# Kernel tuning notes

Hardware: AMD Instinct MI355X
Metric: run time of the kernel (lower is better)

The kernel has to match this reference:

```python
import jax, jax.numpy as jnp
import numpy as np
import math

BS, SEQ = 2048, 50
REL, ETYPE = 6, 4
ATT, HEADS, HEAD = 64, 4, 16
HID, OUT = 128, 64


def setup_inputs() -> dict:
    key = jax.random.key(0)
    ks = jax.random.split(key, 20)
    d = {}
    d['input_seqs'] = jax.random.normal(ks[0], (BS, SEQ, 3, 3, REL), jnp.float32)
    d['input_edge_types'] = jax.random.uniform(ks[1], (BS, SEQ, 3, 3, ETYPE), jnp.float32)
    d['input_masks'] = jax.random.randint(ks[2], (BS, SEQ, 3, 3), 0, 2, jnp.int32)
    def lin(k, fin, fout):
        k1, k2 = jax.random.split(k)
        bound = 1.0 / math.sqrt(fin)
        W = jax.random.uniform(k1, (fout, fin), jnp.float32, -bound, bound)
        b = jax.random.uniform(k2, (fout,), jnp.float32, -bound, bound)
        return W, b
    d['W_fus'], d['b_fus'] = lin(ks[3], REL + ETYPE + 9, 64)
    d['Wk'], d['bk'] = lin(ks[4], REL, ATT)
    d['Wq'], d['bq'] = lin(ks[5], 64, ATT)
    d['Wv'], d['bv'] = lin(ks[6], 64, ATT)
    bound = 1.0 / math.sqrt(HID)
    d['W_ih'] = jax.random.uniform(ks[7], (4 * HID, ATT), jnp.float32, -bound, bound)
    d['W_hh'] = jax.random.uniform(ks[8], (4 * HID, HID), jnp.float32, -bound, bound)
    d['b_ih'] = jax.random.uniform(ks[9], (4 * HID,), jnp.float32, -bound, bound)
    d['b_hh'] = jax.random.uniform(ks[10], (4 * HID,), jnp.float32, -bound, bound)
    d['W_out'], d['b_out'] = lin(ks[11], HID, OUT)
    return d


def _lstm_last(xs, W_ih, W_hh, b_ih, b_hh):
    # xs: (seq, bs, ATT); torch LSTM gate order i,f,g,o. Returns last hidden state.
    b = b_ih + b_hh
    def step(carry, x):
        h, c = carry
        gates = x @ W_ih.T + h @ W_hh.T + b
        i, f, g, o = jnp.split(gates, 4, axis=-1)
        i, f, o = jax.nn.sigmoid(i), jax.nn.sigmoid(f), jax.nn.sigmoid(o)
        g = jnp.tanh(g)
        c = f * c + i * g
        h = o * jnp.tanh(c)
        return (h, c), None
    h0 = jnp.zeros((xs.shape[1], HID), xs.dtype)
    (h, _), _ = jax.lax.scan(step, (h0, h0), xs)
    return h


def reference(input_seqs, input_edge_types, input_masks, W_fus, b_fus, Wk, bk, Wq, bq, Wv, bv, W_ih, W_hh, b_ih, b_hh, W_out, b_out):
    bs, seq = input_seqs.shape[0], input_seqs.shape[1]
    # location one-hot for the 3x3 neighborhood
    loc = jnp.broadcast_to(jnp.eye(9, dtype=input_seqs.dtype).reshape(3, 3, 9), (bs, seq, 3, 3, 9))
    edge_info = jnp.concatenate([input_seqs, input_edge_types, loc], axis=-1)
    edge_info = edge_info @ W_fus.T + b_fus                 # (bs, seq, 3, 3, 64)
    edge_info = edge_info.reshape(bs, seq, 9, 64)
    self_info = input_seqs[:, :, 1, 1]                       # (bs, seq, REL)
    # key from self state (same for all 9 slots), query/value from edge info
    key = (self_info @ Wk.T + bk).reshape(bs, seq, 1, HEADS, HEAD)     # broadcast over 9
    query = (edge_info @ Wq.T + bq).reshape(bs, seq, 9, HEADS, HEAD)
    value = (edge_info @ Wv.T + bv).reshape(bs, seq, 9, HEADS, HEAD)
    # att: dot over head dim -> (bs, seq, heads, 9)
    att = jnp.einsum('bsnhd,bsnhd->bshn', jnp.broadcast_to(key, query.shape), query) / math.sqrt(HEAD)
    mask9 = input_masks.reshape(bs, seq, 1, 9)               # broadcast over heads
    att = jnp.where(mask9 == 0, jnp.float32(-1e10), att)
    att = jax.nn.softmax(att, axis=-1)                       # (bs, seq, heads, 9)
    ctx = jnp.einsum('bshn,bsnhd->bshd', att, value)         # (bs, seq, heads, head)
    ctx = ctx.reshape(bs, seq, ATT).transpose(1, 0, 2)       # (seq, bs, ATT)
    h_last = _lstm_last(ctx, W_ih, W_hh, b_ih, b_hh)         # (bs, HID)
    return h_last @ W_out.T + b_out                          # (bs, OUT)
```

## Files before the change

### kernel.cpp

```cpp
#include <hip/hip_runtime.h>
#include <math.h>

#define BS   2048
#define SEQ  50
#define NPOS (BS * SEQ)

typedef __attribute__((ext_vector_type(8))) short bf16x8;
typedef __attribute__((ext_vector_type(4))) float f32x4;

__device__ __forceinline__ float sigf(float x) { return 1.0f / (1.0f + __expf(-x)); }
__device__ __forceinline__ float tanhfast(float x) {
    float e = __expf(2.0f * x);
    return 1.0f - 2.0f / (e + 1.0f);
}
__device__ __forceinline__ unsigned short bfrn(float x) {
    unsigned int u = __float_as_uint(x);
    u += 0x7FFFu + ((u >> 16) & 1u);
    return (unsigned short)(u >> 16);
}
__device__ __forceinline__ float bf2f(unsigned short h) {
    return __uint_as_float(((unsigned int)h) << 16);
}

#define FMA4(A, X, W) \
    A = fmaf((X).x, (W).x, A); A = fmaf((X).y, (W).y, A); \
    A = fmaf((X).z, (W).z, A); A = fmaf((X).w, (W).w, A);

__device__ float Wvf_d[640];
__device__ float Ce_d[576];
__device__ float Ag_d[280];
__device__ float Bd_d[252];

__global__ __launch_bounds__(512) void prep_all(
    const float* __restrict__ Wih, const float* __restrict__ Whh,
    bf16x8* __restrict__ whF, bf16x8* __restrict__ wiF,
    const float* __restrict__ Wf, const float* __restrict__ bf,
    const float* __restrict__ Wq, const float* __restrict__ bq,
    const float* __restrict__ Wv,
    const float* __restrict__ Wk, const float* __restrict__ bk)
{
    int id = blockIdx.x * 512 + threadIdx.x;
    if (id < 24576) {
        const float* src;
        bf16x8* dst;
        int p;
        if (id < 16384) {
            int l = id & 63, frag = id >> 6;
            p = frag & 1;
            int kc = (frag >> 1) & 3, ti = (frag >> 3) & 3, w = frag >> 5;
            int n  = (w + 8 * ti) * 16 + (l & 15);
            int k0 = kc * 32 + (l >> 4) * 8;
            src = &Whh[n * 128 + k0];
            dst = &whF[frag * 64 + l];
        } else {
            int id2 = id - 16384;
            int l = id2 & 63, frag = id2 >> 6;
            p = frag & 1;
            int kc = (frag >> 1) & 1, tile = frag >> 2;
            int n  = tile * 16 + (l & 15);
            int k0 = kc * 32 + (l >> 4) * 8;
            src = &Wih[n * 64 + k0];
            dst = &wiF[frag * 64 + l];
        }
        bf16x8 v;
        #pragma unroll
        for (int j = 0; j < 8; ++j) {
            float x = src[j];
            unsigned short hi = bfrn(x);
            unsigned short r  = p ? bfrn(x - bf2f(hi)) : hi;
            v[j] = (short)r;
        }
        *dst = v;
        return;
    }
    int i = id - 24576;
    if (i >= 1748) return;
    if (i < 640) {
        int o = i / 10, k = i % 10;
        float s = 0.f;
        #pragma unroll 8
        for (int j = 0; j < 64; ++j) s = fmaf(Wv[o * 64 + j], Wf[j * 19 + k], s);
        Wvf_d[i] = s;
    } else if (i < 1216) {
        int i2 = i - 640;
        int o = i2 / 9, e = i2 % 9;
        float s = 0.f;
        #pragma unroll 8
        for (int j = 0; j < 64; ++j)
            s = fmaf(Wf[j * 19 + 10 + e] + bf[j], Wv[o * 64 + j], s);
        Ce_d[i2] = s;
    } else if (i < 1496) {
        int i3 = i - 1216;
        int h = i3 / 70, rem = i3 % 70, k = rem / 7, j = rem % 7;
        float s = 0.f;
        for (int d = 0; d < 16; ++d) {
            int n = h * 16 + d;
            float Gnk = 0.f;
            #pragma unroll 8
            for (int mm = 0; mm < 64; ++mm)
                Gnk = fmaf(Wq[n * 64 + mm], Wf[mm * 19 + k], Gnk);
            float wkj = (j < 6) ? Wk[n * 6 + j] : bk[n];
            s = fmaf(wkj, Gnk, s);
        }
        Ag_d[i3] = s;
    } else {
        int i4 = i - 1496;
        int e = i4 / 28, rem = i4 % 28, h = rem / 7, j = rem % 7;
        float s = 0.f;
        for (int d = 0; d < 16; ++d) {
            int n = h * 16 + d;
            float Den = bq[n];
            #pragma unroll 8
            for (int mm = 0; mm < 64; ++mm)
                Den = fmaf(Wf[mm * 19 + 10 + e] + bf[mm], Wq[n * 64 + mm], Den);
            float wkj = (j < 6) ? Wk[n * 6 + j] : bk[n];
            s = fmaf(wkj, Den, s);
        }
        Bd_d[i4] = s;
    }
}

__global__ __launch_bounds__(64, 4) void edge_attn_ctx(
    const float* __restrict__ seqs,
    const float* __restrict__ ets,
    const int*   __restrict__ masks,
    const float* __restrict__ bv,
    float* __restrict__ ctx)
{
    const int o   = threadIdx.x;
    const int h_o = o >> 4;
    const int lg  = (o < 40) ? o : 0;
    const int gh  = lg / 10, gk = lg % 10;
    const int la  = (o < 36) ? o : 0;
    const int ah  = la / 9,  ae = la % 9;

    float Agr[7], Bdr[7];
    #pragma unroll
    for (int j = 0; j < 7; ++j) Agr[j] = Ag_d[(gh * 10 + gk) * 7 + j];
    #pragma unroll
    for (int j = 0; j < 7; ++j) Bdr[j] = Bd_d[(ae * 4 + ah) * 7 + j];
    float Wvfr[10];
    #pragma unroll
    for (int k = 0; k < 10; ++k) Wvfr[k] = Wvf_d[o * 10 + k];
    const float bvr = bv[o];
    float Cer[9];
    #pragma unroll
    for (int e = 0; e < 9; ++e) Cer[e] = Ce_d[o * 9 + e] + bvr;

    __shared__ float s_seq[54], s_et[36], s_g[40];
    __shared__ float s_att[36], s_exp[36], s_rbar[40];
    __shared__ int   s_mask[9];

    float r_seq = 0.f, r_et = 0.f; int r_mask = 0;
    {
        int p0 = blockIdx.x;
        if (o < 54) r_seq  = seqs[p0 * 54 + o];
        if (o < 36) r_et   = ets[p0 * 36 + o];
        if (o < 9)  r_mask = masks[p0 * 9 + o];
    }

    for (int p = blockIdx.x; p < NPOS; p += gridDim.x) {
        if (o < 54) s_seq[o]  = r_seq;
        if (o < 36) s_et[o]   = r_et;
        if (o < 9)  s_mask[o] = r_mask;
        __syncthreads();

        {
            int pn = p + gridDim.x;
            if (pn < NPOS) {
                if (o < 54) r_seq  = seqs[pn * 54 + o];
                if (o < 36) r_et   = ets[pn * 36 + o];
                if (o < 9)  r_mask = masks[pn * 9 + o];
            }
        }

        float c0 = s_seq[24], c1 = s_seq[25], c2 = s_seq[26],
              c3 = s_seq[27], c4 = s_seq[28], c5 = s_seq[29];
        float tt = 0.f;
        if (o < 40) {
            float g = Agr[6];
            g = fmaf(c0, Agr[0], g); g = fmaf(c1, Agr[1], g);
            g = fmaf(c2, Agr[2], g); g = fmaf(c3, Agr[3], g);
            g = fmaf(c4, Agr[4], g); g = fmaf(c5, Agr[5], g);
            s_g[o] = g;
        }
        if (o < 36) {
            tt = Bdr[6];
            tt = fmaf(c0, Bdr[0], tt); tt = fmaf(c1, Bdr[1], tt);
            tt = fmaf(c2, Bdr[2], tt); tt = fmaf(c3, Bdr[3], tt);
            tt = fmaf(c4, Bdr[4], tt); tt = fmaf(c5, Bdr[5], tt);
        }
        __syncthreads();

        float a = 0.f;
        if (o < 36) {
            a = tt;
            #pragma unroll
            for (int k = 0; k < 6; ++k) a = fmaf(s_seq[ae * 6 + k], s_g[ah * 10 + k], a);
            #pragma unroll
            for (int k = 0; k < 4; ++k) a = fmaf(s_et[ae * 4 + k], s_g[ah * 10 + 6 + k], a);
            a *= 0.25f;
            if (s_mask[ae] == 0) a = -1.0e10f;
            s_att[o] = a;
        }
        __syncthreads();

        float ex = 0.f;
        if (o < 36) {
            float mx = s_att[ah * 9 + 0];
            #pragma unroll
            for (int e = 1; e < 9; ++e) mx = fmaxf(mx, s_att[ah * 9 + e]);
            ex = __expf(a - mx);
            s_exp[o] = ex;
        }
        __syncthreads();

        if (o < 40) {
            float rb = 0.f;
            #pragma unroll
            for (int e = 0; e < 9; ++e) {
                float x = (gk < 6) ? s_seq[e * 6 + gk] : s_et[e * 4 + (gk - 6)];
                rb = fmaf(s_exp[gh * 9 + e], x, rb);
            }
            s_rbar[o] = rb;
        }
        __syncthreads();

        {
            float ssum = 0.f;
            #pragma unroll
            for (int e = 0; e < 9; ++e) ssum += s_exp[h_o * 9 + e];
            float acc = 0.f;
            #pragma unroll
            for (int k = 0; k < 10; ++k) acc = fmaf(s_rbar[h_o * 10 + k], Wvfr[k], acc);
            #pragma unroll
            for (int e = 0; e < 9; ++e) acc = fmaf(s_exp[h_o * 9 + e], Cer[e], acc);
            ctx[p * 64 + o] = acc * (1.0f / ssum);
        }
        __syncthreads();
    }
}

#define MFMA16(A, B, C) __builtin_amdgcn_mfma_f32_16x16x32_bf16(A, B, C, 0, 0, 0)
#define MM4(F, W0, W1, W2, W3) \
    a0 = MFMA16(F, W0, a0); a1 = MFMA16(F, W1, a1); \
    a2 = MFMA16(F, W2, a2); a3 = MFMA16(F, W3, a3);

#define HPASS \
    MM4(hfh[0], whr[0][0][0], whr[1][0][0], whr[2][0][0], whr[3][0][0]) \
    MM4(hfh[1], whr[0][1][0], whr[1][1][0], whr[2][1][0], whr[3][1][0]) \
    MM4(hfh[2], whr[0][2][0], whr[1][2][0], whr[2][2][0], whr[3][2][0]) \
    MM4(hfh[3], whr[0][3][0], whr[1][3][0], whr[2][3][0], whr[3][3][0]) \
    MM4(hfl[0], whr[0][0][0], whr[1][0][0], whr[2][0][0], whr[3][0][0]) \
    MM4(hfl[1], whr[0][1][0], whr[1][1][0], whr[2][1][0], whr[3][1][0]) \
    MM4(hfl[2], whr[0][2][0], whr[1][2][0], whr[2][2][0], whr[3][2][0]) \
    MM4(hfl[3], whr[0][3][0], whr[1][3][0], whr[2][3][0], whr[3][3][0]) \
    MM4(hfh[0], whr[0][0][1], whr[1][0][1], whr[2][0][1], whr[3][0][1]) \
    MM4(hfh[1], whr[0][1][1], whr[1][1][1], whr[2][1][1], whr[3][1][1]) \
    MM4(hfh[2], whr[0][2][1], whr[1][2][1], whr[2][2][1], whr[3][2][1]) \
    MM4(hfh[3], whr[0][3][1], whr[1][3][1], whr[2][3][1], whr[3][3][1])

#define REDIST_E(ch, g0, g1) { \
    float s2_ = __shfl_xor(ch[2], 32), s3_ = __shfl_xor(ch[3], 32); \
    g0 = lolq ? ch[0] : s2_;  g1 = lolq ? ch[1] : s3_; }
#define REDIST_O(ch, g0, g1) { \
    float s0_ = __shfl_xor(ch[0], 32), s1_ = __shfl_xor(ch[1], 32); \
    g0 = lolq ? s0_ : ch[2];  g1 = lolq ? s1_ : ch[3]; }

#define PWBODY(gi0,gf0,gg0,go0,gi1,gf1,gg1,go1, WB0, WB1) { \
    float i0_ = sigf(gi0 + bi), f0_ = sigf(gf0 + bff); \
    float gA_ = tanhfast(gg0 + bg), o0_ = sigf(go0 + bo); \
    c20 = fmaf(f0_, c20, i0_ * gA_); \
    float hv0_ = o0_ * tanhfast(c20); \
    float i1_ = sigf(gi1 + bi), f1_ = sigf(gf1 + bff); \
    float gB_ = tanhfast(gg1 + bg), o1_ = sigf(go1 + bo); \
    c21 = fmaf(f1_, c21, i1_ * gB_); \
    float hv1_ = o1_ * tanhfast(c21); \
    unsigned short hh0_ = bfrn(hv0_), hh1_ = bfrn(hv1_); \
    unsigned short hl0_ = bfrn(hv0_ - bf2f(hh0_)), hl1_ = bfrn(hv1_ - bf2f(hh1_)); \
    *(unsigned short*)((char*)s_hh + (WB0)) = hh0_; \
    *(unsigned short*)((char*)s_hl + (WB0)) = hl0_; \
    *(unsigned short*)((char*)s_hh + (WB1)) = hh1_; \
    *(unsigned short*)((char*)s_hl + (WB1)) = hl1_; }

__global__ __launch_bounds__(512, 2) void lstm_mfma(
    const float*  __restrict__ ctx,
    const bf16x8* __restrict__ whF,
    const bf16x8* __restrict__ wiFg,
    const float*  __restrict__ b_ih, const float* __restrict__ b_hh,
    const float*  __restrict__ W_out, const float* __restrict__ b_out,
    float* __restrict__ out)
{
    const int t  = threadIdx.x;
    const int w  = t >> 6, l = t & 63;
    const int lm = l & 15, lq = l >> 4;
    const int row0 = blockIdx.x * 8;

    __shared__ bf16x8 s_wi[8192];
    __shared__ unsigned short s_xh[1024], s_xl[1024];
    __shared__ unsigned short s_hh[4096], s_hl[4096];

    for (int i = t; i < 8192; i += 512) s_wi[i] = wiFg[i];
    for (int i = t; i < 1024; i += 512) { s_xh[i] = 0; s_xl[i] = 0; }
    for (int i = t; i < 4096; i += 512) { s_hh[i] = 0; s_hl[i] = 0; }

    bf16x8 whr[4][4][2];
    #pragma unroll
    for (int ti = 0; ti < 4; ++ti)
        #pragma unroll
        for (int kc = 0; kc < 4; ++kc)
            #pragma unroll
            for (int p = 0; p < 2; ++p)
                whr[ti][kc][p] = whF[(((w * 4 + ti) * 4 + kc) * 2 + p) * 64 + l];

    const int m = w * 16 + lm;
    const float bi  = b_ih[m]       + b_hh[m];
    const float bff = b_ih[128 + m] + b_hh[128 + m];
    const float bg  = b_ih[256 + m] + b_hh[256 + m];
    const float bo  = b_ih[384 + m] + b_hh[384 + m];

    const int  urb  = ((lq & 1) << 2) | (lq & 2);
    const bool lolq = (lq < 2);
    float c20 = 0.f, c21 = 0.f;

    const int xrow  = t >> 5;
    const int xl32  = t & 31;
    const int srow  = xrow & 7;
    const int spair = xrow >> 3;
    const float2* ctx2 = (const float2*)ctx;
    const int xbase = (row0 + srow) * SEQ + spair;
    const int xwb   = xrow * 128 + ((4 * xl32) ^ ((xrow & 7) << 4));
    const int swzr  = (lm & 7) << 4;
    const int hwb_m = 32 * w + 2 * lm;
    const int wb0e = 4096 + (8 + urb) * 256 + (hwb_m ^ (urb << 4));
    const int wb1e = 4096 + (9 + urb) * 256 + (hwb_m ^ ((urb + 1) << 4));
    const int wb0o = urb * 256 + (hwb_m ^ (urb << 4));
    const int wb1o = (urb + 1) * 256 + (hwb_m ^ ((urb + 1) << 4));

    float2 xv = ctx2[xbase * 32 + xl32];

    for (int u = 0; u < SEQ / 2; ++u) {
        {
            unsigned short xh0 = bfrn(xv.x), xh1 = bfrn(xv.y);
            unsigned short xl0 = bfrn(xv.x - bf2f(xh0)), xl1 = bfrn(xv.y - bf2f(xh1));
            *(unsigned int*)((char*)s_xh + xwb) = (unsigned int)xh0 | ((unsigned int)xh1 << 16);
            *(unsigned int*)((char*)s_xl + xwb) = (unsigned int)xl0 | ((unsigned int)xl1 << 16);
        }
        __syncthreads();

        float2 xvn = make_float2(0.f, 0.f);
        if (u + 1 < SEQ / 2) xvn = ctx2[(xbase + 2 * u + 2) * 32 + xl32];

        bf16x8 hfh[4], hfl[4];
        if (u > 0) {
            #pragma unroll
            for (int kc = 0; kc < 4; ++kc) {
                int b = lm * 256 + ((kc * 64 + lq * 16) ^ swzr);
                hfh[kc] = *(const bf16x8*)((const char*)s_hh + b);
                hfl[kc] = *(const bf16x8*)((const char*)s_hl + b);
            }
        }
        bf16x8 xfh[2], xfl[2];
        #pragma unroll
        for (int kc = 0; kc < 2; ++kc) {
            int b = lm * 128 + ((kc * 64 + lq * 16) ^ swzr);
            xfh[kc] = *(const bf16x8*)((const char*)s_xh + b);
            xfl[kc] = *(const bf16x8*)((const char*)s_xl + b);
        }

        f32x4 a0 = {0.f,0.f,0.f,0.f}, a1 = a0, a2 = a0, a3 = a0;

        if (u > 0) { HPASS }

        #pragma unroll
        for (int kc = 0; kc < 2; ++kc) {
            bf16x8 wihi[4], wilo[4];
            #pragma unroll
            for (int ti = 0; ti < 4; ++ti) {
                int base = (((w + 8 * ti) * 2 + kc) * 2) * 64 + l;
                wihi[ti] = s_wi[base];
                wilo[ti] = s_wi[base + 64];
            }
            MM4(xfh[kc], wihi[0], wihi[1], wihi[2], wihi[3])
            MM4(xfl[kc], wihi[0], wihi[1], wihi[2], wihi[3])
            MM4(xfh[kc], wilo[0], wilo[1], wilo[2], wilo[3])
        }

        {
            float gi0, gi1, gf0, gf1, gg0, gg1, go0, go1;
            REDIST_E(a0, gi0, gi1)
            REDIST_E(a1, gf0, gf1)
            REDIST_E(a2, gg0, gg1)
            REDIST_E(a3, go0, go1)
            PWBODY(gi0, gf0, gg0, go0, gi1, gf1, gg1, go1, wb0e, wb1e)
        }

        __syncthreads();
        #pragma unroll
        for (int kc = 0; kc < 4; ++kc) {
            int b = 4096 + lm * 256 + ((kc * 64 + lq * 16) ^ swzr);
            hfh[kc] = *(const bf16x8*)((const char*)s_hh + b);
            hfl[kc] = *(const bf16x8*)((const char*)s_hl + b);
        }
        HPASS

        {
            float gi0, gi1, gf0, gf1, gg0, gg1, go0, go1;
            REDIST_O(a0, gi0, gi1)
            REDIST_O(a1, gf0, gf1)
            REDIST_O(a2, gg0, gg1)
            REDIST_O(a3, go0, go1)
            PWBODY(gi0, gf0, gg0, go0, gi1, gf1, gg1, go1, wb0o, wb1o)
        }
        xv = xvn;
    }
    __syncthreads();

    {
        const int row = t >> 5;
        if (row < 8) {
            const int j0 = t & 31, j1 = (t & 31) + 32;
            const int rswz = (row & 7) << 4;
            float accA = b_out[j0], accB = b_out[j1];
            #pragma unroll
            for (int kq = 0; kq < 16; ++kq) {
                int b = row * 256 + ((kq * 16) ^ rswz);
                bf16x8 hh8 = *(const bf16x8*)((const char*)s_hh + b);
                bf16x8 hl8 = *(const bf16x8*)((const char*)s_hl + b);
                #pragma unroll
                for (int e = 0; e < 8; ++e) {
                    float h = bf2f((unsigned short)hh8[e]) + bf2f((unsigned short)hl8[e]);
                    int k = kq * 8 + e;
                    accA = fmaf(h, W_out[j0 * 128 + k], accA);
                    accB = fmaf(h, W_out[j1 * 128 + k], accB);
                }
            }
            out[(row0 + row) * 64 + j0] = accA;
            out[(row0 + row) * 64 + j1] = accB;
        }
    }
}

extern "C" void kernel_launch(void* const* d_in, const int* in_sizes, int n_in,
                              void* d_out, int out_size, void* d_ws, size_t ws_size,
                              hipStream_t stream) {
    (void)in_sizes; (void)n_in; (void)out_size; (void)ws_size;
    const float* seqs  = (const float*)d_in[0];
    const float* ets   = (const float*)d_in[1];
    const int*   masks = (const int*)d_in[2];
    const float* Wf  = (const float*)d_in[3];
    const float* bf  = (const float*)d_in[4];
    const float* Wk  = (const float*)d_in[5];
    const float* bk  = (const float*)d_in[6];
    const float* Wq  = (const float*)d_in[7];
    const float* bq  = (const float*)d_in[8];
    const float* Wv  = (const float*)d_in[9];
    const float* bv  = (const float*)d_in[10];
    const float* Wih = (const float*)d_in[11];
    const float* Whh = (const float*)d_in[12];
    const float* bih = (const float*)d_in[13];
    const float* bhh = (const float*)d_in[14];
    const float* Wo  = (const float*)d_in[15];
    const float* bo  = (const float*)d_in[16];

    char* ws = (char*)d_ws;
    bf16x8* whF = (bf16x8*)(ws);
    bf16x8* wiF = (bf16x8*)(ws + 262144);
    float*  ctx = (float*) (ws + 262144 + 131072);

    hipLaunchKernelGGL(prep_all, dim3(52), dim3(512), 0, stream,
                       Wih, Whh, whF, wiF, Wf, bf, Wq, bq, Wv, Wk, bk);
    hipLaunchKernelGGL(edge_attn_ctx, dim3(4096), dim3(64), 0, stream,
                       seqs, ets, masks, bv, ctx);
    hipLaunchKernelGGL(lstm_mfma, dim3(256), dim3(512), 0, stream,
                       ctx, whF, wiF, bih, bhh, Wo, bo, (float*)d_out);
}
```

Baseline: 281.5 us.

## Replace LDS staging and barriers in edge attention with wave shuffles

```diff
diff --git a/kernel.cpp b/kernel.cpp
--- a/kernel.cpp
+++ b/kernel.cpp
@@ -39,8 +39,11 @@
     const float* __restrict__ Wv,
     const float* __restrict__ Wk, const float* __restrict__ bk)
 {
-    int id = blockIdx.x * 512 + threadIdx.x;
-    if (id < 24576) {
+    __shared__ float sG[640];
+    __shared__ float sD[576];
+
+    if (blockIdx.x < 48) {
+        int id = blockIdx.x * 512 + threadIdx.x;
         const float* src;
         bf16x8* dst;
         int p;
@@ -73,50 +76,70 @@
         *dst = v;
         return;
     }
-    int i = id - 24576;
-    if (i >= 1748) return;
-    if (i < 640) {
-        int o = i / 10, k = i % 10;
-        float s = 0.f;
-        #pragma unroll 8
-        for (int j = 0; j < 64; ++j) s = fmaf(Wv[o * 64 + j], Wf[j * 19 + k], s);
-        Wvf_d[i] = s;
-    } else if (i < 1216) {
-        int i2 = i - 640;
-        int o = i2 / 9, e = i2 % 9;
-        float s = 0.f;
-        #pragma unroll 8
-        for (int j = 0; j < 64; ++j)
-            s = fmaf(Wf[j * 19 + 10 + e] + bf[j], Wv[o * 64 + j], s);
-        Ce_d[i2] = s;
-    } else if (i < 1496) {
-        int i3 = i - 1216;
-        int h = i3 / 70, rem = i3 % 70, k = rem / 7, j = rem % 7;
-        float s = 0.f;
-        for (int d = 0; d < 16; ++d) {
-            int n = h * 16 + d;
-            float Gnk = 0.f;
+
+    if (blockIdx.x < 51) {
+        int i = (blockIdx.x - 48) * 512 + threadIdx.x;
+        if (i >= 1216) return;
+        if (i < 640) {
+            int o = i / 10, k = i % 10;
+            float s = 0.f;
             #pragma unroll 8
-            for (int mm = 0; mm < 64; ++mm)
-                Gnk = fmaf(Wq[n * 64 + mm], Wf[mm * 19 + k], Gnk);
-            float wkj = (j < 6) ? Wk[n * 6 + j] : bk[n];
-            s = fmaf(wkj, Gnk, s);
-        }
-        Ag_d[i3] = s;
-    } else {
-        int i4 = i - 1496;
-        int e = i4 / 28, rem = i4 % 28, h = rem / 7, j = rem % 7;
-        float s = 0.f;
-        for (int d = 0; d < 16; ++d) {
-            int n = h * 16 + d;
-            float Den = bq[n];
+            for (int j = 0; j < 64; ++j) s = fmaf(Wv[o * 64 + j], Wf[j * 19 + k], s);
+            Wvf_d[i] = s;
+        } else {
+            int i2 = i - 640;
+            int o = i2 / 9, e = i2 % 9;
+            float s = 0.f;
             #pragma unroll 8
-            for (int mm = 0; mm < 64; ++mm)
-                Den = fmaf(Wf[mm * 19 + 10 + e] + bf[mm], Wq[n * 64 + mm], Den);
-            float wkj = (j < 6) ? Wk[n * 6 + j] : bk[n];
-            s = fmaf(wkj, Den, s);
-        }
-        Bd_d[i4] = s;
+            for (int j = 0; j < 64; ++j)
+                s = fmaf(Wf[j * 19 + 10 + e] + bf[j], Wv[o * 64 + j], s);
+            Ce_d[i2] = s;
+        }
+        return;
+    }
+
+    const int t = threadIdx.x;
+    for (int i = t; i < 1216; i += 512) {
+        if (i < 640) {
+            int n = i / 10, k = i % 10;
+            float s = 0.f;
+            #pragma unroll 8
+            for (int j = 0; j < 64; ++j) s = fmaf(Wq[n * 64 + j], Wf[j * 19 + k], s);
+            sG[i] = s;
+        } else {
+            int i2 = i - 640;
+            int e = i2 >> 6, n = i2 & 63;
+            float s = bq[n];
+            #pragma unroll 8
+            for (int j = 0; j < 64; ++j)
+                s = fmaf(Wf[j * 19 + 10 + e] + bf[j], Wq[n * 64 + j], s);
+            sD[i2] = s;
+        }
+    }
+    __syncthreads();
+    for (int i = t; i < 532; i += 512) {
+        if (i < 280) {
+            int h = i / 70, rem = i % 70, k = rem / 7, jj = rem % 7;
+            float s = 0.f;
+            #pragma unroll
+            for (int d = 0; d < 16; ++d) {
+                int n = h * 16 + d;
+                float wkj = (jj < 6) ? Wk[n * 6 + jj] : bk[n];
+                s = fmaf(wkj, sG[n * 10 + k], s);
+            }
+            Ag_d[i] = s;
+        } else {
+            int i4 = i - 280;
+            int e = i4 / 28, rem = i4 % 28, h = rem / 7, jj = rem % 7;
+            float s = 0.f;
+            #pragma unroll
+            for (int d = 0; d < 16; ++d) {
+                int n = h * 16 + d;
+                float wkj = (jj < 6) ? Wk[n * 6 + jj] : bk[n];
+                s = fmaf(wkj, sD[e * 64 + n], s);
+            }
+            Bd_d[i4] = s;
+        }
     }
 }
 
@@ -127,18 +150,17 @@
     const float* __restrict__ bv,
     float* __restrict__ ctx)
 {
-    const int o   = threadIdx.x;
-    const int h_o = o >> 4;
-    const int lg  = (o < 40) ? o : 0;
-    const int gh  = lg / 10, gk = lg % 10;
-    const int la  = (o < 36) ? o : 0;
-    const int ah  = la / 9,  ae = la % 9;
-
+    const int o = threadIdx.x;
+    const int j = o & 15, h = o >> 4;
+    const int j6 = j * 6, j4 = j * 4;
+
+    const int jA = (j < 10) ? j : 9;
+    const int jB = (j < 9)  ? j : 8;
     float Agr[7], Bdr[7];
     #pragma unroll
-    for (int j = 0; j < 7; ++j) Agr[j] = Ag_d[(gh * 10 + gk) * 7 + j];
+    for (int q = 0; q < 7; ++q) Agr[q] = Ag_d[(h * 10 + jA) * 7 + q];
     #pragma unroll
-    for (int j = 0; j < 7; ++j) Bdr[j] = Bd_d[(ae * 4 + ah) * 7 + j];
+    for (int q = 0; q < 7; ++q) Bdr[q] = Bd_d[(jB * 4 + h) * 7 + q];
     float Wvfr[10];
     #pragma unroll
     for (int k = 0; k < 10; ++k) Wvfr[k] = Wvf_d[o * 10 + k];
@@ -147,23 +169,17 @@
     #pragma unroll
     for (int e = 0; e < 9; ++e) Cer[e] = Ce_d[o * 9 + e] + bvr;
 
-    __shared__ float s_seq[54], s_et[36], s_g[40];
-    __shared__ float s_att[36], s_exp[36], s_rbar[40];
-    __shared__ int   s_mask[9];
+    const bool selR = (j < 6);
+    const int jc = selR ? j : 0;
+    const int jm = (j >= 6) ? (j - 6) : 0;
 
     float r_seq = 0.f, r_et = 0.f; int r_mask = 0;
-    {
-        int p0 = blockIdx.x;
-        if (o < 54) r_seq  = seqs[p0 * 54 + o];
-        if (o < 36) r_et   = ets[p0 * 36 + o];
-        if (o < 9)  r_mask = masks[p0 * 9 + o];
-    }
+    if (o < 54) r_seq  = seqs[blockIdx.x * 54 + o];
+    if (o < 36) r_et   = ets[blockIdx.x * 36 + o];
+    if (o < 9)  r_mask = masks[blockIdx.x * 9 + o];
 
     for (int p = blockIdx.x; p < NPOS; p += gridDim.x) {
-        if (o < 54) s_seq[o]  = r_seq;
-        if (o < 36) s_et[o]   = r_et;
-        if (o < 9)  s_mask[o] = r_mask;
-        __syncthreads();
+        const float cs = r_seq, cet = r_et; const int cm = r_mask;
 
         {
             int pn = p + gridDim.x;
@@ -174,70 +190,62 @@
             }
         }
 
-        float c0 = s_seq[24], c1 = s_seq[25], c2 = s_seq[26],
-              c3 = s_seq[27], c4 = s_seq[28], c5 = s_seq[29];
-        float tt = 0.f;
-        if (o < 40) {
-            float g = Agr[6];
-            g = fmaf(c0, Agr[0], g); g = fmaf(c1, Agr[1], g);
-            g = fmaf(c2, Agr[2], g); g = fmaf(c3, Agr[3], g);
-            g = fmaf(c4, Agr[4], g); g = fmaf(c5, Agr[5], g);
-            s_g[o] = g;
-        }
-        if (o < 36) {
-            tt = Bdr[6];
-            tt = fmaf(c0, Bdr[0], tt); tt = fmaf(c1, Bdr[1], tt);
-            tt = fmaf(c2, Bdr[2], tt); tt = fmaf(c3, Bdr[3], tt);
-            tt = fmaf(c4, Bdr[4], tt); tt = fmaf(c5, Bdr[5], tt);
-        }
-        __syncthreads();
-
-        float a = 0.f;
-        if (o < 36) {
-            a = tt;
-            #pragma unroll
-            for (int k = 0; k < 6; ++k) a = fmaf(s_seq[ae * 6 + k], s_g[ah * 10 + k], a);
-            #pragma unroll
-            for (int k = 0; k < 4; ++k) a = fmaf(s_et[ae * 4 + k], s_g[ah * 10 + 6 + k], a);
-            a *= 0.25f;
-            if (s_mask[ae] == 0) a = -1.0e10f;
-            s_att[o] = a;
-        }
-        __syncthreads();
-
-        float ex = 0.f;
-        if (o < 36) {
-            float mx = s_att[ah * 9 + 0];
-            #pragma unroll
-            for (int e = 1; e < 9; ++e) mx = fmaxf(mx, s_att[ah * 9 + e]);
-            ex = __expf(a - mx);
-            s_exp[o] = ex;
-        }
-        __syncthreads();
-
-        if (o < 40) {
-            float rb = 0.f;
-            #pragma unroll
-            for (int e = 0; e < 9; ++e) {
-                float x = (gk < 6) ? s_seq[e * 6 + gk] : s_et[e * 4 + (gk - 6)];
-                rb = fmaf(s_exp[gh * 9 + e], x, rb);
-            }
-            s_rbar[o] = rb;
-        }
-        __syncthreads();
-
-        {
-            float ssum = 0.f;
-            #pragma unroll
-            for (int e = 0; e < 9; ++e) ssum += s_exp[h_o * 9 + e];
-            float acc = 0.f;
-            #pragma unroll
-            for (int k = 0; k < 10; ++k) acc = fmaf(s_rbar[h_o * 10 + k], Wvfr[k], acc);
-            #pragma unroll
-            for (int e = 0; e < 9; ++e) acc = fmaf(s_exp[h_o * 9 + e], Cer[e], acc);
-            ctx[p * 64 + o] = acc * (1.0f / ssum);
-        }
-        __syncthreads();
+        float c0 = __shfl(cs, 24), c1 = __shfl(cs, 25), c2 = __shfl(cs, 26),
+              c3 = __shfl(cs, 27), c4 = __shfl(cs, 28), c5 = __shfl(cs, 29);
+
+        float g = Agr[6];
+        g = fmaf(c0, Agr[0], g); g = fmaf(c1, Agr[1], g);
+        g = fmaf(c2, Agr[2], g); g = fmaf(c3, Agr[3], g);
+        g = fmaf(c4, Agr[4], g); g = fmaf(c5, Agr[5], g);
+        float tt = Bdr[6];
+        tt = fmaf(c0, Bdr[0], tt); tt = fmaf(c1, Bdr[1], tt);
+        tt = fmaf(c2, Bdr[2], tt); tt = fmaf(c3, Bdr[3], tt);
+        tt = fmaf(c4, Bdr[4], tt); tt = fmaf(c5, Bdr[5], tt);
+
+        float a = tt;
+        #pragma unroll
+        for (int k = 0; k < 6; ++k)
+            a = fmaf(__shfl(cs, j6 + k), __shfl(g, k, 16), a);
+        #pragma unroll
+        for (int k = 6; k < 10; ++k)
+            a = fmaf(__shfl(cet, j4 + (k - 6)), __shfl(g, k, 16), a);
+        a *= 0.25f;
+        int mk = __shfl(cm, j);
+        a = (mk == 0) ? -1.0e10f : a;
+        if (j >= 9) a = -3.0e38f;
+
+        float mx = a;
+        mx = fmaxf(mx, __shfl_xor(mx, 1, 16));
+        mx = fmaxf(mx, __shfl_xor(mx, 2, 16));
+        mx = fmaxf(mx, __shfl_xor(mx, 4, 16));
+        mx = fmaxf(mx, __shfl_xor(mx, 8, 16));
+        float ex = __expf(a - mx);
+        float ss = ex;
+        ss += __shfl_xor(ss, 1, 16);
+        ss += __shfl_xor(ss, 2, 16);
+        ss += __shfl_xor(ss, 4, 16);
+        ss += __shfl_xor(ss, 8, 16);
+
+        float exe[9];
+        #pragma unroll
+        for (int e = 0; e < 9; ++e) exe[e] = __shfl(ex, e, 16);
+
+        float rb = 0.f;
+        #pragma unroll
+        for (int e = 0; e < 9; ++e) {
+            float xa = __shfl(cs,  e * 6 + jc);
+            float xb = __shfl(cet, e * 4 + jm);
+            rb = fmaf(exe[e], selR ? xa : xb, rb);
+        }
+
+        float acc = 0.f;
+        #pragma unroll
+        for (int k = 0; k < 10; ++k)
+            acc = fmaf(__shfl(rb, k, 16), Wvfr[k], acc);
+        #pragma unroll
+        for (int e = 0; e < 9; ++e)
+            acc = fmaf(exe[e], Cer[e], acc);
+        ctx[p * 64 + o] = acc * (1.0f / ss);
     }
 }
 
```

Result: slower. 290.8 us (+3.3%).
